# Performance work log

Hardware: AMD Instinct MI355X
Metric: run time of the kernel (lower is better)

Reference implementation:

```python
import jax, jax.numpy as jnp
import numpy as np

N_NODES = 100000
N_EDGES = 200000
IN_FEATS = 1024
H_FEATS = 512
N_HEADS = 4
HEAD_DIM = H_FEATS // N_HEADS  # 128
N_CLASSES = 2983
BATCH = 1024


def setup_inputs() -> dict:
    key = jax.random.key(0)
    ks = jax.random.split(key, 24)
    x = jax.random.normal(ks[0], (N_NODES, IN_FEATS), jnp.float32)
    e1_src = jax.random.randint(ks[1], (N_EDGES,), 0, N_NODES)
    e1_dst = jax.random.randint(ks[2], (N_EDGES,), 0, N_NODES)
    e2_src = jax.random.randint(ks[3], (N_EDGES,), 0, N_NODES)
    e2_dst = jax.random.randint(ks[4], (N_EDGES,), 0, N_NODES)

    def lin_w(k, fin, fout):
        return jax.random.normal(k, (fin, fout), jnp.float32) * np.float32(1.0 / np.sqrt(fin))

    def att_w(k):
        return jax.random.normal(k, (N_HEADS, HEAD_DIM), jnp.float32) * np.float32(0.1)

    inp = dict(x=x, e1_src=e1_src, e1_dst=e1_dst, e2_src=e2_src, e2_dst=e2_dst,
               batch_size=BATCH)
    # layer 0 (in_feats -> h_feats), one GATConv per edge type
    inp["w0a"] = lin_w(ks[5], IN_FEATS, H_FEATS); inp["as0a"] = att_w(ks[6]); inp["ad0a"] = att_w(ks[7]); inp["b0a"] = jnp.zeros((H_FEATS,), jnp.float32)
    inp["w0b"] = lin_w(ks[8], IN_FEATS, H_FEATS); inp["as0b"] = att_w(ks[9]); inp["ad0b"] = att_w(ks[10]); inp["b0b"] = jnp.zeros((H_FEATS,), jnp.float32)
    # layer 1 (h_feats -> h_feats)
    inp["w1a"] = lin_w(ks[11], H_FEATS, H_FEATS); inp["as1a"] = att_w(ks[12]); inp["ad1a"] = att_w(ks[13]); inp["b1a"] = jnp.zeros((H_FEATS,), jnp.float32)
    inp["w1b"] = lin_w(ks[14], H_FEATS, H_FEATS); inp["as1b"] = att_w(ks[15]); inp["ad1b"] = att_w(ks[16]); inp["b1b"] = jnp.zeros((H_FEATS,), jnp.float32)
    # classification head
    inp["lin_w"] = lin_w(ks[17], H_FEATS, N_CLASSES)
    inp["lin_b"] = jnp.zeros((N_CLASSES,), jnp.float32)
    return inp


def gat_conv(x, src, dst, W, a_src, a_dst, b):
    """PyG GATConv (add_self_loops=False, concat=True, attn negative_slope=0.2)."""
    h = (x @ W).reshape(-1, N_HEADS, HEAD_DIM)          # [N, H, C]
    alpha_src = jnp.einsum('nhc,hc->nh', h, a_src)       # [N, H]
    alpha_dst = jnp.einsum('nhc,hc->nh', h, a_dst)       # [N, H]
    e = jax.nn.leaky_relu(alpha_src[src] + alpha_dst[dst], 0.2)   # [E, H]
    # segment softmax over incoming edges of each destination node
    m = jax.ops.segment_max(e, dst, num_segments=N_NODES)          # [N, H]
    ex = jnp.exp(e - m[dst])
    denom = jax.ops.segment_sum(ex, dst, num_segments=N_NODES)     # [N, H]
    alpha = ex / denom[dst]                                        # [E, H]
    msg = alpha[:, :, None] * h[src]                               # [E, H, C]
    out = jax.ops.segment_sum(msg, dst, num_segments=N_NODES)      # [N, H, C]
    return out.reshape(-1, N_HEADS * HEAD_DIM) + b


def reference(x, e1_src, e1_dst, e2_src, e2_dst, batch_size,
              w0a, as0a, ad0a, b0a, w0b, as0b, ad0b, b0b,
              w1a, as1a, ad1a, b1a, w1b, as1b, ad1b, b1b,
              lin_w, lin_b):
    # layer 0: HeteroConv sums per-edge-type GATConv outputs on 'paper'
    h1 = gat_conv(x, e1_src, e1_dst, w0a, as0a, ad0a, b0a) \
       + gat_conv(x, e2_src, e2_dst, w0b, as0b, ad0b, b0b)
    h1 = jax.nn.leaky_relu(h1, 0.01)   # F.leaky_relu default slope; dropout is identity in eval
    # layer 1
    h2 = gat_conv(h1, e1_src, e1_dst, w1a, as1a, ad1a, b1a) \
       + gat_conv(h1, e2_src, e2_dst, w1b, as1b, ad1b, b1b)
    # classification head on the seed nodes
    return h2[:batch_size] @ lin_w + lin_b
```

## Files before the change

### kernel.cpp

```cpp
#include <hip/hip_runtime.h>

#define N_NODES 100000
#define N_EDGES 200000
#define IN_FEATS 1024
#define H_FEATS 512
#define N_HEADS 4
#define HEAD_DIM 128
#define N_CLASSES 2983
#define BATCH 1024

typedef __attribute__((ext_vector_type(8))) short short8;
typedef __attribute__((ext_vector_type(4))) float floatx4;

typedef __attribute__((address_space(1))) void global_as_void;
typedef __attribute__((address_space(3))) void lds_as_void;

__device__ __forceinline__ float bf2f(unsigned short u) {
    union { unsigned int i; float f; } x; x.i = ((unsigned int)u) << 16; return x.f;
}
__device__ __forceinline__ unsigned short f2bf(float f) {
    union { float f; unsigned int i; } x; x.f = f;
    unsigned int r = x.i + 0x7FFFu + ((x.i >> 16) & 1u);
    return (unsigned short)(r >> 16);
}
__device__ __forceinline__ void load_lds16(const void* g, void* l) {
    __builtin_amdgcn_global_load_lds((const global_as_void*)g, (lds_as_void*)l, 16, 0, 0);
}

__global__ __launch_bounds__(256, 3)
void gemm_kernel(const void* __restrict__ Ain, int a_fp32, int a_dense,
                 const unsigned short* __restrict__ BT,
                 void* __restrict__ Cout, const float* __restrict__ bias,
                 const float* __restrict__ att_s, const float* __restrict__ att_d,
                 const float* __restrict__ att_s2, const float* __restrict__ att_d2,
                 float* __restrict__ asrc, float* __restrict__ adst,
                 const int* __restrict__ rowlist, const int* __restrict__ countp,
                 int M, int N, int n_tiles, int K, int out_bf16)
{
    __shared__ __attribute__((aligned(16))) unsigned short As[128 * 32];
    __shared__ __attribute__((aligned(16))) unsigned short Bs[128 * 32];
    const int tid  = threadIdx.x;
    const int lane = tid & 63;
    const int wave = tid >> 6;
    const int bid = blockIdx.x;
    int mt, nt;
    if (n_tiles == 8) {
        int k8 = bid & 7, j = bid >> 3;
        nt = j & 7;
        mt = k8 + ((j >> 3) << 3);
    } else {
        mt = bid / n_tiles;
        nt = bid - mt * n_tiles;
    }
    const int m0 = mt * 128;
    const int n0 = nt * 128;
    int Mv = M;
    if (countp) Mv = countp[0];
    if (m0 >= Mv) return;
    const int wr = (wave >> 1) * 64;
    const int wc = (wave & 1) * 64;
    const int lm = lane & 15;
    const int quad = lane >> 4;

    auto arow = [&](int r) -> int {
        int gr = m0 + r; if (gr > Mv - 1) gr = Mv - 1;
        if (rowlist && !a_dense) gr = rowlist[gr];
        return gr;
    };

    floatx4 acc[4][4];
#pragma unroll
    for (int i = 0; i < 4; i++)
#pragma unroll
        for (int j = 0; j < 4; j++) acc[i][j] = (floatx4)0.0f;

    for (int k0 = 0; k0 < K; k0 += 32) {
        __syncthreads();
        if (a_fp32) {
            int row = tid >> 2;
            int slot = tid & 3;
#pragma unroll
            for (int p = 0; p < 2; p++) {
                int r = p * 64 + row;
                int gr = arow(r);
                int gc = (slot ^ ((r >> 1) & 3)) * 8;
                const float* ap = (const float*)Ain + (size_t)gr * K + k0 + gc;
                floatx4 f0 = *(const floatx4*)ap;
                floatx4 f1 = *(const floatx4*)(ap + 4);
                short8 v;
                v[0] = (short)f2bf(f0[0]); v[1] = (short)f2bf(f0[1]);
                v[2] = (short)f2bf(f0[2]); v[3] = (short)f2bf(f0[3]);
                v[4] = (short)f2bf(f1[0]); v[5] = (short)f2bf(f1[1]);
                v[6] = (short)f2bf(f1[2]); v[7] = (short)f2bf(f1[3]);
                *(short8*)&As[r * 32 + slot * 8] = v;
            }
        } else {
#pragma unroll
            for (int i = 0; i < 2; i++) {
                int r = wave * 32 + i * 16 + (lane >> 2);
                int gr = arow(r);
                int gc = ((lane & 3) ^ ((r >> 1) & 3)) * 8;
                load_lds16((const unsigned short*)Ain + (size_t)gr * K + k0 + gc,
                           (char*)As + (size_t)(wave * 2 + i) * 1024);
            }
        }
#pragma unroll
        for (int i = 0; i < 2; i++) {
            int r = wave * 32 + i * 16 + (lane >> 2);
            int gn = n0 + r; if (gn > N - 1) gn = N - 1;
            int gc = ((lane & 3) ^ ((r >> 1) & 3)) * 8;
            load_lds16(BT + (size_t)gn * K + k0 + gc,
                       (char*)Bs + (size_t)(wave * 2 + i) * 1024);
        }
        __syncthreads();
        short8 af[4], bfr[4];
#pragma unroll
        for (int i = 0; i < 4; i++) {
            int ra = wr + i * 16 + lm;
            af[i] = *(const short8*)&As[ra * 32 + ((quad ^ ((ra >> 1) & 3)) << 3)];
            int rb = wc + i * 16 + lm;
            bfr[i] = *(const short8*)&Bs[rb * 32 + ((quad ^ ((rb >> 1) & 3)) << 3)];
        }
#pragma unroll
        for (int i = 0; i < 4; i++)
#pragma unroll
            for (int j = 0; j < 4; j++)
                acc[i][j] = __builtin_amdgcn_mfma_f32_16x16x32_bf16(af[i], bfr[j], acc[i][j], 0, 0, 0);
    }

    if (att_s) {
        const int h = nt;
        const float* wsp = (h < 4) ? att_s : att_s2;
        const float* wdp = (h < 4) ? att_d : att_d2;
        const int hh = h & 3;
#pragma unroll
        for (int i = 0; i < 4; i++) {
#pragma unroll
            for (int r = 0; r < 4; r++) {
                float ss = 0.f, sd = 0.f;
#pragma unroll
                for (int j = 0; j < 4; j++) {
                    int c = wc + j * 16 + lm;
                    ss += acc[i][j][r] * wsp[hh * HEAD_DIM + c];
                    sd += acc[i][j][r] * wdp[hh * HEAD_DIM + c];
                }
#pragma unroll
                for (int off = 1; off < 16; off <<= 1) {
                    ss += __shfl_xor(ss, off);
                    sd += __shfl_xor(sd, off);
                }
                int grl = m0 + wr + i * 16 + quad * 4 + r;
                if (lm == 0 && grl < Mv) {
                    int gr = rowlist ? rowlist[grl] : grl;
                    atomicAdd(&asrc[(size_t)gr * 8 + h], ss);
                    atomicAdd(&adst[(size_t)gr * 8 + h], sd);
                }
            }
        }
    }

#pragma unroll
    for (int i = 0; i < 4; i++) {
        int grb = wr + i * 16 + quad * 4;
#pragma unroll
        for (int j = 0; j < 4; j++) {
            int gc = n0 + wc + j * 16 + lm;
            if (gc < N) {
#pragma unroll
                for (int r = 0; r < 4; r++) {
                    int grl = m0 + grb + r;
                    if (grl < Mv) {
                        int gr = rowlist ? rowlist[grl] : grl;
                        float v = acc[i][j][r];
                        if (out_bf16) {
                            ((unsigned short*)Cout)[(size_t)gr * N + gc] = f2bf(v);
                        } else {
                            float b = bias ? bias[gc] : 0.0f;
                            ((float*)Cout)[(size_t)gr * N + gc] = v + b;
                        }
                    }
                }
            }
        }
    }
}

__global__ void cvt_rows_kernel(const float* __restrict__ X, const int* __restrict__ list,
                                const int* __restrict__ countp, unsigned short* __restrict__ Y)
{
    int i = blockIdx.x * 2 + (threadIdx.x >> 7);
    if (i >= countp[0]) return;
    int col = (threadIdx.x & 127) * 8;
    const floatx4* xp = (const floatx4*)(X + (size_t)list[i] * IN_FEATS + col);
    floatx4 f0 = xp[0], f1 = xp[1];
    short8 v;
    v[0] = (short)f2bf(f0[0]); v[1] = (short)f2bf(f0[1]);
    v[2] = (short)f2bf(f0[2]); v[3] = (short)f2bf(f0[3]);
    v[4] = (short)f2bf(f1[0]); v[5] = (short)f2bf(f1[1]);
    v[6] = (short)f2bf(f1[2]); v[7] = (short)f2bf(f1[3]);
    *(short8*)(Y + (size_t)i * IN_FEATS + col) = v;
}

__global__ void hist_kernel(const int* __restrict__ dst, int* __restrict__ cnt, int E)
{
    int e = blockIdx.x * blockDim.x + threadIdx.x;
    if (e < E) atomicAdd(&cnt[dst[e]], 1);
}

__global__ void scan1_kernel(const int* __restrict__ cnt, int* __restrict__ partial,
                             int* __restrict__ chunksum, int n)
{
    __shared__ int sm[256];
    int t = threadIdx.x;
    int i = blockIdx.x * 256 + t;
    int v = (i < n) ? cnt[i] : 0;
    sm[t] = v; __syncthreads();
    int val = v;
#pragma unroll
    for (int off = 1; off < 256; off <<= 1) {
        int u = (t >= off) ? sm[t - off] : 0;
        __syncthreads();
        val += u; sm[t] = val;
        __syncthreads();
    }
    if (i < n) partial[i] = val - v;
    if (t == 255) chunksum[blockIdx.x] = val;
}

__global__ void scan2_kernel(int* __restrict__ chunksum, int n)
{
    __shared__ int sm[512];
    int t = threadIdx.x;
    int v = (t < n) ? chunksum[t] : 0;
    sm[t] = v; __syncthreads();
    int val = v;
#pragma unroll
    for (int off = 1; off < 512; off <<= 1) {
        int u = (t >= off) ? sm[t - off] : 0;
        __syncthreads();
        val += u; sm[t] = val;
        __syncthreads();
    }
    if (t < n) chunksum[t] = val - v;
}

__global__ void scan3_kernel(const int* __restrict__ partial, const int* __restrict__ chunksum,
                             int* __restrict__ rowptr, int* __restrict__ cursor, int n, int E)
{
    int i = blockIdx.x * 256 + threadIdx.x;
    if (i < n) {
        int r = partial[i] + chunksum[i >> 8];
        rowptr[i] = r;
        cursor[i] = r;
    }
    if (i == 0) rowptr[n] = E;
}

__global__ void fill_kernel(const int* __restrict__ src, const int* __restrict__ dst,
                            int* __restrict__ cursor, int* __restrict__ srcs_sorted, int E)
{
    int e = blockIdx.x * blockDim.x + threadIdx.x;
    if (e < E) {
        int p = atomicAdd(&cursor[dst[e]], 1);
        srcs_sorted[p] = src[e];
    }
}

__global__ void mark1_kernel(const int* __restrict__ rowptr1, const int* __restrict__ srcs1,
                             const int* __restrict__ rowptr2, const int* __restrict__ srcs2,
                             int* __restrict__ flag, int E)
{
    int e = blockIdx.x * blockDim.x + threadIdx.x;
    if (e >= E) return;
    if (e < BATCH) flag[e] = 1;
    if (e < rowptr1[BATCH]) flag[srcs1[e]] = 1;
    if (e < rowptr2[BATCH]) flag[srcs2[e]] = 1;
}

__global__ void mark0_kernel(const int* __restrict__ e1s, const int* __restrict__ e1d,
                             const int* __restrict__ e2s, const int* __restrict__ e2d,
                             const int* __restrict__ flag1, int* __restrict__ flag0,
                             int E, int Nn)
{
    int i = blockIdx.x * blockDim.x + threadIdx.x;
    if (i < E) {
        if (flag1[e1d[i]]) flag0[e1s[i]] = 1;
        if (flag1[e2d[i]]) flag0[e2s[i]] = 1;
    }
    if (i < Nn && flag1[i]) flag0[i] = 1;
}

__global__ void compact_kernel(const int* __restrict__ flag, const int* __restrict__ partial,
                               const int* __restrict__ chunksum, int* __restrict__ list,
                               int* __restrict__ countp, int n)
{
    int i = blockIdx.x * 256 + threadIdx.x;
    if (i >= n) return;
    int pos = partial[i] + chunksum[i >> 8];
    if (flag[i]) list[pos] = i;
    if (i == n - 1) countp[0] = pos + flag[i];
}

__global__ void gather2_kernel(const int* __restrict__ rowptr1, const int* __restrict__ srcs1,
                               const int* __restrict__ rowptr2, const int* __restrict__ srcs2,
                               const float* __restrict__ asrc, const float* __restrict__ adst,
                               const unsigned short* __restrict__ H,
                               const float* __restrict__ b1, const float* __restrict__ b2,
                               const int* __restrict__ dlist, const int* __restrict__ dcountp,
                               unsigned short* __restrict__ Out, int ndst, int do_lrelu)
{
    int i = blockIdx.x * 4 + (threadIdx.x >> 6);
    int nd = dcountp ? dcountp[0] : ndst;
    if (i >= nd) return;
    int d = dlist ? dlist[i] : i;
    int lane = threadIdx.x & 63;
    int head = lane >> 4;
    int col = lane * 8;
    float r[8], acc[8];
    {
        int beg = rowptr1[d], end = rowptr1[d + 1];
        float ad = adst[(size_t)d * 8 + head];
        float den = 0.f;
#pragma unroll
        for (int k = 0; k < 8; k++) acc[k] = 0.f;
        for (int j = beg; j < end; j++) {
            int s = srcs1[j];
            float v = asrc[(size_t)s * 8 + head] + ad;
            v = v > 0.f ? v : 0.2f * v;
            float ex = expf(v);
            den += ex;
            short8 hv = *(const short8*)(H + (size_t)s * 1024 + col);
#pragma unroll
            for (int k = 0; k < 8; k++) acc[k] += ex * bf2f((unsigned short)hv[k]);
        }
        float inv = den > 0.f ? 1.f / den : 0.f;
#pragma unroll
        for (int k = 0; k < 8; k++) r[k] = acc[k] * inv;
    }
    {
        int beg = rowptr2[d], end = rowptr2[d + 1];
        float ad = adst[(size_t)d * 8 + 4 + head];
        float den = 0.f;
#pragma unroll
        for (int k = 0; k < 8; k++) acc[k] = 0.f;
        for (int j = beg; j < end; j++) {
            int s = srcs2[j];
            float v = asrc[(size_t)s * 8 + 4 + head] + ad;
            v = v > 0.f ? v : 0.2f * v;
            float ex = expf(v);
            den += ex;
            short8 hv = *(const short8*)(H + (size_t)s * 1024 + 512 + col);
#pragma unroll
            for (int k = 0; k < 8; k++) acc[k] += ex * bf2f((unsigned short)hv[k]);
        }
        float inv = den > 0.f ? 1.f / den : 0.f;
#pragma unroll
        for (int k = 0; k < 8; k++) r[k] += acc[k] * inv;
    }
    short8 o;
#pragma unroll
    for (int k = 0; k < 8; k++) {
        float f = r[k] + b1[col + k] + b2[col + k];
        if (do_lrelu) f = f > 0.f ? f : 0.01f * f;
        o[k] = (short)f2bf(f);
    }
    *(short8*)(Out + (size_t)i * 512 + col) = o;
}

__global__ void transpose_conv_kernel(const float* __restrict__ W, unsigned short* __restrict__ WT,
                                      int K, int N)
{
    int idx = blockIdx.x * blockDim.x + threadIdx.x;
    if (idx >= K * N) return;
    int n = idx / K, k = idx - n * K;
    WT[idx] = f2bf(W[(size_t)k * N + n]);
}

extern "C" void kernel_launch(void* const* d_in, const int* in_sizes, int n_in,
                              void* d_out, int out_size, void* d_ws, size_t ws_size,
                              hipStream_t stream)
{
    const float* x    = (const float*)d_in[0];
    const int* e1s    = (const int*)d_in[1];
    const int* e1d    = (const int*)d_in[2];
    const int* e2s    = (const int*)d_in[3];
    const int* e2d    = (const int*)d_in[4];
    const float* w0a  = (const float*)d_in[6];
    const float* as0a = (const float*)d_in[7];
    const float* ad0a = (const float*)d_in[8];
    const float* b0a  = (const float*)d_in[9];
    const float* w0b  = (const float*)d_in[10];
    const float* as0b = (const float*)d_in[11];
    const float* ad0b = (const float*)d_in[12];
    const float* b0b  = (const float*)d_in[13];
    const float* w1a  = (const float*)d_in[14];
    const float* as1a = (const float*)d_in[15];
    const float* ad1a = (const float*)d_in[16];
    const float* b1a  = (const float*)d_in[17];
    const float* w1b  = (const float*)d_in[18];
    const float* as1b = (const float*)d_in[19];
    const float* ad1b = (const float*)d_in[20];
    const float* b1b  = (const float*)d_in[21];
    const float* linw = (const float*)d_in[22];
    const float* linb = (const float*)d_in[23];
    float* out = (float*)d_out;
    (void)in_sizes; (void)n_in; (void)out_size;

    char* ws = (char*)d_ws;
    size_t off = 0;
    auto carve = [&](size_t bytes) -> void* {
        void* p = ws + off; off += (bytes + 255) & ~(size_t)255; return p;
    };
    unsigned short* WT0 = (unsigned short*)carve((size_t)2 * H_FEATS * IN_FEATS * 2);
    unsigned short* WT1 = (unsigned short*)carve((size_t)2 * H_FEATS * H_FEATS * 2);
    unsigned short* WTl = (unsigned short*)carve((size_t)N_CLASSES * H_FEATS * 2);
    unsigned short* Hbf = (unsigned short*)carve((size_t)N_NODES * 1024 * 2);
    unsigned short* H1c = (unsigned short*)carve((size_t)N_NODES * H_FEATS * 2);
    unsigned short* h2s = (unsigned short*)carve((size_t)BATCH * H_FEATS * 2);
    float* asrc = (float*)carve((size_t)N_NODES * 8 * 4);
    float* adst = (float*)carve((size_t)N_NODES * 8 * 4);
    int* rowptr1 = (int*)carve((size_t)(N_NODES + 1) * 4);
    int* rowptr2 = (int*)carve((size_t)(N_NODES + 1) * 4);
    int* srcs1   = (int*)carve((size_t)N_EDGES * 4);
    int* srcs2   = (int*)carve((size_t)N_EDGES * 4);
    int* cnt     = (int*)carve((size_t)N_NODES * 4);
    int* partial = (int*)carve((size_t)N_NODES * 4);
    int* chunksum= (int*)carve((size_t)512 * 4);
    int* flag1   = (int*)carve((size_t)N_NODES * 4);
    int* flag0   = (int*)carve((size_t)N_NODES * 4);
    int* list1   = (int*)carve((size_t)N_NODES * 4);
    int* list0   = (int*)carve((size_t)N_NODES * 4);
    int* count1  = (int*)carve(256);
    int* count0  = (int*)carve(256);
    unsigned short* xc = nullptr;
    {
        size_t need = (size_t)N_NODES * IN_FEATS * 2;
        if (off + need <= ws_size) xc = (unsigned short*)carve(need);
    }

    const int NCHUNK = (N_NODES + 255) / 256;
    const int MT8 = (((N_NODES + 127) / 128) + 7) & ~7;

    {
        int t0 = IN_FEATS * H_FEATS;
        transpose_conv_kernel<<<(t0 + 255) / 256, 256, 0, stream>>>(w0a, WT0, IN_FEATS, H_FEATS);
        transpose_conv_kernel<<<(t0 + 255) / 256, 256, 0, stream>>>(w0b, WT0 + (size_t)H_FEATS * IN_FEATS, IN_FEATS, H_FEATS);
        int t1 = H_FEATS * H_FEATS;
        transpose_conv_kernel<<<(t1 + 255) / 256, 256, 0, stream>>>(w1a, WT1, H_FEATS, H_FEATS);
        transpose_conv_kernel<<<(t1 + 255) / 256, 256, 0, stream>>>(w1b, WT1 + (size_t)H_FEATS * H_FEATS, H_FEATS, H_FEATS);
        int t2 = H_FEATS * N_CLASSES;
        transpose_conv_kernel<<<(t2 + 255) / 256, 256, 0, stream>>>(linw, WTl, H_FEATS, N_CLASSES);
    }

    auto build_csr = [&](const int* src, const int* dst, int* rowptr, int* srcs_sorted) {
        hipMemsetAsync(cnt, 0, (size_t)N_NODES * 4, stream);
        hist_kernel<<<(N_EDGES + 255) / 256, 256, 0, stream>>>(dst, cnt, N_EDGES);
        scan1_kernel<<<NCHUNK, 256, 0, stream>>>(cnt, partial, chunksum, N_NODES);
        scan2_kernel<<<1, 512, 0, stream>>>(chunksum, NCHUNK);
        scan3_kernel<<<NCHUNK, 256, 0, stream>>>(partial, chunksum, rowptr, cnt, N_NODES, N_EDGES);
        fill_kernel<<<(N_EDGES + 255) / 256, 256, 0, stream>>>(src, dst, cnt, srcs_sorted, N_EDGES);
    };
    build_csr(e1s, e1d, rowptr1, srcs1);
    build_csr(e2s, e2d, rowptr2, srcs2);

    hipMemsetAsync(flag1, 0, (size_t)N_NODES * 4, stream);
    mark1_kernel<<<(N_EDGES + 255) / 256, 256, 0, stream>>>(rowptr1, srcs1, rowptr2, srcs2, flag1, N_EDGES);
    scan1_kernel<<<NCHUNK, 256, 0, stream>>>(flag1, partial, chunksum, N_NODES);
    scan2_kernel<<<1, 512, 0, stream>>>(chunksum, NCHUNK);
    compact_kernel<<<NCHUNK, 256, 0, stream>>>(flag1, partial, chunksum, list1, count1, N_NODES);

    hipMemsetAsync(flag0, 0, (size_t)N_NODES * 4, stream);
    mark0_kernel<<<(N_EDGES + 255) / 256, 256, 0, stream>>>(e1s, e1d, e2s, e2d, flag1, flag0, N_EDGES, N_NODES);
    scan1_kernel<<<NCHUNK, 256, 0, stream>>>(flag0, partial, chunksum, N_NODES);
    scan2_kernel<<<1, 512, 0, stream>>>(chunksum, NCHUNK);
    compact_kernel<<<NCHUNK, 256, 0, stream>>>(flag0, partial, chunksum, list0, count0, N_NODES);

    if (xc) {
        cvt_rows_kernel<<<(N_NODES + 1) / 2, 256, 0, stream>>>(x, list0, count0, xc);
    }

    hipMemsetAsync(asrc, 0, (size_t)N_NODES * 8 * 4, stream);
    hipMemsetAsync(adst, 0, (size_t)N_NODES * 8 * 4, stream);
    if (xc) {
        gemm_kernel<<<MT8 * 8, 256, 0, stream>>>(xc, 0, 1, WT0, Hbf, nullptr,
                                                 as0a, ad0a, as0b, ad0b, asrc, adst,
                                                 list0, count0,
                                                 N_NODES, 1024, 8, IN_FEATS, 1);
    } else {
        gemm_kernel<<<MT8 * 8, 256, 0, stream>>>(x, 1, 0, WT0, Hbf, nullptr,
                                                 as0a, ad0a, as0b, ad0b, asrc, adst,
                                                 list0, count0,
                                                 N_NODES, 1024, 8, IN_FEATS, 1);
    }
    gather2_kernel<<<(N_NODES + 3) / 4, 256, 0, stream>>>(rowptr1, srcs1, rowptr2, srcs2,
                                                          asrc, adst, Hbf, b0a, b0b,
                                                          list1, count1,
                                                          H1c, N_NODES, 1);

    hipMemsetAsync(asrc, 0, (size_t)N_NODES * 8 * 4, stream);
    hipMemsetAsync(adst, 0, (size_t)N_NODES * 8 * 4, stream);
    gemm_kernel<<<MT8 * 8, 256, 0, stream>>>(H1c, 0, 1, WT1, Hbf, nullptr,
                                             as1a, ad1a, as1b, ad1b, asrc, adst,
                                             list1, count1,
                                             N_NODES, 1024, 8, H_FEATS, 1);
    gather2_kernel<<<(BATCH + 3) / 4, 256, 0, stream>>>(rowptr1, srcs1, rowptr2, srcs2,
                                                        asrc, adst, Hbf, b1a, b1b,
                                                        nullptr, nullptr,
                                                        h2s, BATCH, 0);

    const int HN_T = (N_CLASSES + 127) / 128;
    gemm_kernel<<<(BATCH / 128) * HN_T, 256, 0, stream>>>(h2s, 0, 0, WTl, out, linb,
                                                          nullptr, nullptr, nullptr, nullptr,
                                                          nullptr, nullptr, nullptr, nullptr,
                                                          BATCH, N_CLASSES, HN_T, H_FEATS, 0);
}
```

Measured before the change: 850.9 us.

## Merge CSR builds and frontier compaction, replace attention atomics with LDS reduction

Builds both edge-type CSRs in one combined histogram/scan/fill pass and computes both frontier flag sets in a single scan and compaction. The five weight transposes become three batched launches, and gather and convert kernels switch to fixed-size grid-stride grids. In the GEMM, per-thread load pointers are hoisted out of the K loop. The attention-logit atomics are replaced with an LDS reduction followed by plain stores, which removes the asrc/adst memsets. The goal is fewer launches and memsets and less atomic traffic, at the cost of a larger single-block scan and an extra barrier in the GEMM epilogue.

```diff
diff --git a/kernel.cpp b/kernel.cpp
--- a/kernel.cpp
+++ b/kernel.cpp
@@ -39,15 +39,15 @@
 {
     __shared__ __attribute__((aligned(16))) unsigned short As[128 * 32];
     __shared__ __attribute__((aligned(16))) unsigned short Bs[128 * 32];
+    __shared__ float attbuf[128][4];
     const int tid  = threadIdx.x;
     const int lane = tid & 63;
     const int wave = tid >> 6;
     const int bid = blockIdx.x;
     int mt, nt;
     if (n_tiles == 8) {
-        int k8 = bid & 7, j = bid >> 3;
-        nt = j & 7;
-        mt = k8 + ((j >> 3) << 3);
+        mt = (bid & 7) + ((bid >> 6) << 3);
+        nt = (bid >> 3) & 7;
     } else {
         mt = bid / n_tiles;
         nt = bid - mt * n_tiles;
@@ -68,6 +68,35 @@
         return gr;
     };
 
+    const float* a_fp[2];
+    const unsigned short* a_bf[2];
+    char* a_lds[2];
+    const unsigned short* b_bf[2];
+    char* b_lds[2];
+    if (a_fp32) {
+        int row = tid >> 2, slot = tid & 3;
+#pragma unroll
+        for (int p = 0; p < 2; p++) {
+            int r = p * 64 + row;
+            a_fp[p] = (const float*)Ain + (size_t)arow(r) * K + (slot ^ ((r >> 1) & 3)) * 8;
+        }
+    } else {
+#pragma unroll
+        for (int i = 0; i < 2; i++) {
+            int r = wave * 32 + i * 16 + (lane >> 2);
+            a_bf[i] = (const unsigned short*)Ain + (size_t)arow(r) * K
+                    + ((lane & 3) ^ ((r >> 1) & 3)) * 8;
+            a_lds[i] = (char*)As + (size_t)(wave * 2 + i) * 1024;
+        }
+    }
+#pragma unroll
+    for (int i = 0; i < 2; i++) {
+        int r = wave * 32 + i * 16 + (lane >> 2);
+        int gn = n0 + r; if (gn > N - 1) gn = N - 1;
+        b_bf[i] = BT + (size_t)gn * K + ((lane & 3) ^ ((r >> 1) & 3)) * 8;
+        b_lds[i] = (char*)Bs + (size_t)(wave * 2 + i) * 1024;
+    }
+
     floatx4 acc[4][4];
 #pragma unroll
     for (int i = 0; i < 4; i++)
@@ -77,16 +106,12 @@
     for (int k0 = 0; k0 < K; k0 += 32) {
         __syncthreads();
         if (a_fp32) {
-            int row = tid >> 2;
-            int slot = tid & 3;
+            int row = tid >> 2, slot = tid & 3;
 #pragma unroll
             for (int p = 0; p < 2; p++) {
                 int r = p * 64 + row;
-                int gr = arow(r);
-                int gc = (slot ^ ((r >> 1) & 3)) * 8;
-                const float* ap = (const float*)Ain + (size_t)gr * K + k0 + gc;
-                floatx4 f0 = *(const floatx4*)ap;
-                floatx4 f1 = *(const floatx4*)(ap + 4);
+                floatx4 f0 = *(const floatx4*)(a_fp[p] + k0);
+                floatx4 f1 = *(const floatx4*)(a_fp[p] + k0 + 4);
                 short8 v;
                 v[0] = (short)f2bf(f0[0]); v[1] = (short)f2bf(f0[1]);
                 v[2] = (short)f2bf(f0[2]); v[3] = (short)f2bf(f0[3]);
@@ -96,22 +121,12 @@
             }
         } else {
 #pragma unroll
-            for (int i = 0; i < 2; i++) {
-                int r = wave * 32 + i * 16 + (lane >> 2);
-                int gr = arow(r);
-                int gc = ((lane & 3) ^ ((r >> 1) & 3)) * 8;
-                load_lds16((const unsigned short*)Ain + (size_t)gr * K + k0 + gc,
-                           (char*)As + (size_t)(wave * 2 + i) * 1024);
-            }
-        }
-#pragma unroll
-        for (int i = 0; i < 2; i++) {
-            int r = wave * 32 + i * 16 + (lane >> 2);
-            int gn = n0 + r; if (gn > N - 1) gn = N - 1;
-            int gc = ((lane & 3) ^ ((r >> 1) & 3)) * 8;
-            load_lds16(BT + (size_t)gn * K + k0 + gc,
-                       (char*)Bs + (size_t)(wave * 2 + i) * 1024);
-        }
+            for (int i = 0; i < 2; i++)
+                load_lds16(a_bf[i] + k0, a_lds[i]);
+        }
+#pragma unroll
+        for (int i = 0; i < 2; i++)
+            load_lds16(b_bf[i] + k0, b_lds[i]);
         __syncthreads();
         short8 af[4], bfr[4];
 #pragma unroll
@@ -133,6 +148,7 @@
         const float* wsp = (h < 4) ? att_s : att_s2;
         const float* wdp = (h < 4) ? att_d : att_d2;
         const int hh = h & 3;
+        const int half2 = (wc >> 6) * 2;
 #pragma unroll
         for (int i = 0; i < 4; i++) {
 #pragma unroll
@@ -149,12 +165,20 @@
                     ss += __shfl_xor(ss, off);
                     sd += __shfl_xor(sd, off);
                 }
-                int grl = m0 + wr + i * 16 + quad * 4 + r;
-                if (lm == 0 && grl < Mv) {
-                    int gr = rowlist ? rowlist[grl] : grl;
-                    atomicAdd(&asrc[(size_t)gr * 8 + h], ss);
-                    atomicAdd(&adst[(size_t)gr * 8 + h], sd);
+                if (lm == 0) {
+                    int rl = wr + i * 16 + quad * 4 + r;
+                    attbuf[rl][half2]     = ss;
+                    attbuf[rl][half2 + 1] = sd;
                 }
+            }
+        }
+        __syncthreads();
+        if (tid < 128) {
+            int grl = m0 + tid;
+            if (grl < Mv) {
+                int gr = rowlist ? rowlist[grl] : grl;
+                asrc[(size_t)gr * 8 + h] = attbuf[tid][0] + attbuf[tid][2];
+                adst[(size_t)gr * 8 + h] = attbuf[tid][1] + attbuf[tid][3];
             }
         }
     }
@@ -188,23 +212,28 @@
 __global__ void cvt_rows_kernel(const float* __restrict__ X, const int* __restrict__ list,
                                 const int* __restrict__ countp, unsigned short* __restrict__ Y)
 {
-    int i = blockIdx.x * 2 + (threadIdx.x >> 7);
-    if (i >= countp[0]) return;
+    int n0 = countp[0];
     int col = (threadIdx.x & 127) * 8;
-    const floatx4* xp = (const floatx4*)(X + (size_t)list[i] * IN_FEATS + col);
-    floatx4 f0 = xp[0], f1 = xp[1];
-    short8 v;
-    v[0] = (short)f2bf(f0[0]); v[1] = (short)f2bf(f0[1]);
-    v[2] = (short)f2bf(f0[2]); v[3] = (short)f2bf(f0[3]);
-    v[4] = (short)f2bf(f1[0]); v[5] = (short)f2bf(f1[1]);
-    v[6] = (short)f2bf(f1[2]); v[7] = (short)f2bf(f1[3]);
-    *(short8*)(Y + (size_t)i * IN_FEATS + col) = v;
-}
-
-__global__ void hist_kernel(const int* __restrict__ dst, int* __restrict__ cnt, int E)
+    for (int i = blockIdx.x * 2 + (threadIdx.x >> 7); i < n0; i += gridDim.x * 2) {
+        const floatx4* xp = (const floatx4*)(X + (size_t)list[i] * IN_FEATS + col);
+        floatx4 f0 = xp[0], f1 = xp[1];
+        short8 v;
+        v[0] = (short)f2bf(f0[0]); v[1] = (short)f2bf(f0[1]);
+        v[2] = (short)f2bf(f0[2]); v[3] = (short)f2bf(f0[3]);
+        v[4] = (short)f2bf(f1[0]); v[5] = (short)f2bf(f1[1]);
+        v[6] = (short)f2bf(f1[2]); v[7] = (short)f2bf(f1[3]);
+        *(short8*)(Y + (size_t)i * IN_FEATS + col) = v;
+    }
+}
+
+__global__ void hist2_kernel(const int* __restrict__ e1d, const int* __restrict__ e2d,
+                             int* __restrict__ cnt2, int E)
 {
     int e = blockIdx.x * blockDim.x + threadIdx.x;
-    if (e < E) atomicAdd(&cnt[dst[e]], 1);
+    if (e < E) {
+        atomicAdd(&cnt2[e1d[e]], 1);
+        atomicAdd(&cnt2[N_NODES + e2d[e]], 1);
+    }
 }
 
 __global__ void scan1_kernel(const int* __restrict__ cnt, int* __restrict__ partial,
@@ -229,13 +258,13 @@
 
 __global__ void scan2_kernel(int* __restrict__ chunksum, int n)
 {
-    __shared__ int sm[512];
+    __shared__ int sm[1024];
     int t = threadIdx.x;
     int v = (t < n) ? chunksum[t] : 0;
     sm[t] = v; __syncthreads();
     int val = v;
 #pragma unroll
-    for (int off = 1; off < 512; off <<= 1) {
+    for (int off = 1; off < 1024; off <<= 1) {
         int u = (t >= off) ? sm[t - off] : 0;
         __syncthreads();
         val += u; sm[t] = val;
@@ -244,37 +273,40 @@
     if (t < n) chunksum[t] = val - v;
 }
 
-__global__ void scan3_kernel(const int* __restrict__ partial, const int* __restrict__ chunksum,
-                             int* __restrict__ rowptr, int* __restrict__ cursor, int n, int E)
+__global__ void scan3c_kernel(const int* __restrict__ partial, const int* __restrict__ chunksum,
+                              int* __restrict__ rowptrc, int* __restrict__ cursor, int n, int Etot)
 {
     int i = blockIdx.x * 256 + threadIdx.x;
     if (i < n) {
         int r = partial[i] + chunksum[i >> 8];
-        rowptr[i] = r;
+        rowptrc[i] = r;
         cursor[i] = r;
     }
-    if (i == 0) rowptr[n] = E;
-}
-
-__global__ void fill_kernel(const int* __restrict__ src, const int* __restrict__ dst,
-                            int* __restrict__ cursor, int* __restrict__ srcs_sorted, int E)
+    if (i == 0) rowptrc[n] = Etot;
+}
+
+__global__ void fill2_kernel(const int* __restrict__ e1s, const int* __restrict__ e1d,
+                             const int* __restrict__ e2s, const int* __restrict__ e2d,
+                             int* __restrict__ cursor, int* __restrict__ srcsc, int E)
 {
     int e = blockIdx.x * blockDim.x + threadIdx.x;
     if (e < E) {
-        int p = atomicAdd(&cursor[dst[e]], 1);
-        srcs_sorted[p] = src[e];
-    }
-}
-
-__global__ void mark1_kernel(const int* __restrict__ rowptr1, const int* __restrict__ srcs1,
-                             const int* __restrict__ rowptr2, const int* __restrict__ srcs2,
-                             int* __restrict__ flag, int E)
+        int p = atomicAdd(&cursor[e1d[e]], 1);
+        srcsc[p] = e1s[e];
+        int q = atomicAdd(&cursor[N_NODES + e2d[e]], 1);
+        srcsc[q] = e2s[e];
+    }
+}
+
+__global__ void mark1_kernel(const int* __restrict__ e1s, const int* __restrict__ e1d,
+                             const int* __restrict__ e2s, const int* __restrict__ e2d,
+                             int* __restrict__ flag1, int E)
 {
     int e = blockIdx.x * blockDim.x + threadIdx.x;
     if (e >= E) return;
-    if (e < BATCH) flag[e] = 1;
-    if (e < rowptr1[BATCH]) flag[srcs1[e]] = 1;
-    if (e < rowptr2[BATCH]) flag[srcs2[e]] = 1;
+    if (e < BATCH) flag1[e] = 1;
+    if (e1d[e] < BATCH) flag1[e1s[e]] = 1;
+    if (e2d[e] < BATCH) flag1[e2s[e]] = 1;
 }
 
 __global__ void mark0_kernel(const int* __restrict__ e1s, const int* __restrict__ e1d,
@@ -290,90 +322,98 @@
     if (i < Nn && flag1[i]) flag0[i] = 1;
 }
 
-__global__ void compact_kernel(const int* __restrict__ flag, const int* __restrict__ partial,
-                               const int* __restrict__ chunksum, int* __restrict__ list,
-                               int* __restrict__ countp, int n)
+__global__ void compactF_kernel(const int* __restrict__ flag, const int* __restrict__ partial,
+                                const int* __restrict__ chunksum,
+                                int* __restrict__ list1, int* __restrict__ list0,
+                                int* __restrict__ count1, int* __restrict__ count0)
 {
     int i = blockIdx.x * 256 + threadIdx.x;
-    if (i >= n) return;
+    if (i >= 2 * N_NODES) return;
+    int total1 = partial[N_NODES] + chunksum[N_NODES >> 8];
     int pos = partial[i] + chunksum[i >> 8];
-    if (flag[i]) list[pos] = i;
-    if (i == n - 1) countp[0] = pos + flag[i];
-}
-
-__global__ void gather2_kernel(const int* __restrict__ rowptr1, const int* __restrict__ srcs1,
-                               const int* __restrict__ rowptr2, const int* __restrict__ srcs2,
+    if (i < N_NODES) {
+        if (flag[i]) list1[pos] = i;
+        if (i == 0) count1[0] = total1;
+    } else {
+        if (flag[i]) list0[pos - total1] = i - N_NODES;
+        if (i == 2 * N_NODES - 1) count0[0] = pos + flag[i] - total1;
+    }
+}
+
+__global__ void gather2_kernel(const int* __restrict__ rowptrc, const int* __restrict__ srcsc,
                                const float* __restrict__ asrc, const float* __restrict__ adst,
                                const unsigned short* __restrict__ H,
                                const float* __restrict__ b1, const float* __restrict__ b2,
                                const int* __restrict__ dlist, const int* __restrict__ dcountp,
                                unsigned short* __restrict__ Out, int ndst, int do_lrelu)
 {
-    int i = blockIdx.x * 4 + (threadIdx.x >> 6);
     int nd = dcountp ? dcountp[0] : ndst;
-    if (i >= nd) return;
-    int d = dlist ? dlist[i] : i;
     int lane = threadIdx.x & 63;
     int head = lane >> 4;
     int col = lane * 8;
-    float r[8], acc[8];
-    {
-        int beg = rowptr1[d], end = rowptr1[d + 1];
-        float ad = adst[(size_t)d * 8 + head];
-        float den = 0.f;
-#pragma unroll
-        for (int k = 0; k < 8; k++) acc[k] = 0.f;
-        for (int j = beg; j < end; j++) {
-            int s = srcs1[j];
-            float v = asrc[(size_t)s * 8 + head] + ad;
-            v = v > 0.f ? v : 0.2f * v;
-            float ex = expf(v);
-            den += ex;
-            short8 hv = *(const short8*)(H + (size_t)s * 1024 + col);
-#pragma unroll
-            for (int k = 0; k < 8; k++) acc[k] += ex * bf2f((unsigned short)hv[k]);
-        }
-        float inv = den > 0.f ? 1.f / den : 0.f;
-#pragma unroll
-        for (int k = 0; k < 8; k++) r[k] = acc[k] * inv;
-    }
-    {
-        int beg = rowptr2[d], end = rowptr2[d + 1];
-        float ad = adst[(size_t)d * 8 + 4 + head];
-        float den = 0.f;
-#pragma unroll
-        for (int k = 0; k < 8; k++) acc[k] = 0.f;
-        for (int j = beg; j < end; j++) {
-            int s = srcs2[j];
-            float v = asrc[(size_t)s * 8 + 4 + head] + ad;
-            v = v > 0.f ? v : 0.2f * v;
-            float ex = expf(v);
-            den += ex;
-            short8 hv = *(const short8*)(H + (size_t)s * 1024 + 512 + col);
-#pragma unroll
-            for (int k = 0; k < 8; k++) acc[k] += ex * bf2f((unsigned short)hv[k]);
-        }
-        float inv = den > 0.f ? 1.f / den : 0.f;
-#pragma unroll
-        for (int k = 0; k < 8; k++) r[k] += acc[k] * inv;
-    }
-    short8 o;
-#pragma unroll
-    for (int k = 0; k < 8; k++) {
-        float f = r[k] + b1[col + k] + b2[col + k];
-        if (do_lrelu) f = f > 0.f ? f : 0.01f * f;
-        o[k] = (short)f2bf(f);
-    }
-    *(short8*)(Out + (size_t)i * 512 + col) = o;
-}
-
-__global__ void transpose_conv_kernel(const float* __restrict__ W, unsigned short* __restrict__ WT,
-                                      int K, int N)
-{
-    int idx = blockIdx.x * blockDim.x + threadIdx.x;
-    if (idx >= K * N) return;
-    int n = idx / K, k = idx - n * K;
-    WT[idx] = f2bf(W[(size_t)k * N + n]);
+    for (int i = blockIdx.x * 4 + (threadIdx.x >> 6); i < nd; i += gridDim.x * 4) {
+        int d = dlist ? dlist[i] : i;
+        float r[8], acc[8];
+        {
+            int beg = rowptrc[d], end = rowptrc[d + 1];
+            float ad = adst[(size_t)d * 8 + head];
+            float den = 0.f;
+#pragma unroll
+            for (int k = 0; k < 8; k++) acc[k] = 0.f;
+            for (int j = beg; j < end; j++) {
+                int s = srcsc[j];
+                float v = asrc[(size_t)s * 8 + head] + ad;
+                v = v > 0.f ? v : 0.2f * v;
+                float ex = expf(v);
+                den += ex;
+                short8 hv = *(const short8*)(H + (size_t)s * 1024 + col);
+#pragma unroll
+                for (int k = 0; k < 8; k++) acc[k] += ex * bf2f((unsigned short)hv[k]);
+            }
+            float inv = den > 0.f ? 1.f / den : 0.f;
+#pragma unroll
+            for (int k = 0; k < 8; k++) r[k] = acc[k] * inv;
+        }
+        {
+            int beg = rowptrc[N_NODES + d], end = rowptrc[N_NODES + d + 1];
+            float ad = adst[(size_t)d * 8 + 4 + head];
+            float den = 0.f;
+#pragma unroll
+            for (int k = 0; k < 8; k++) acc[k] = 0.f;
+            for (int j = beg; j < end; j++) {
+                int s = srcsc[j];
+                float v = asrc[(size_t)s * 8 + 4 + head] + ad;
+                v = v > 0.f ? v : 0.2f * v;
+                float ex = expf(v);
+                den += ex;
+                short8 hv = *(const short8*)(H + (size_t)s * 1024 + 512 + col);
+#pragma unroll
+                for (int k = 0; k < 8; k++) acc[k] += ex * bf2f((unsigned short)hv[k]);
+            }
+            float inv = den > 0.f ? 1.f / den : 0.f;
+#pragma unroll
+            for (int k = 0; k < 8; k++) r[k] += acc[k] * inv;
+        }
+        short8 o;
+#pragma unroll
+        for (int k = 0; k < 8; k++) {
+            float f = r[k] + b1[col + k] + b2[col + k];
+            if (do_lrelu) f = f > 0.f ? f : 0.01f * f;
+            o[k] = (short)f2bf(f);
+        }
+        *(short8*)(Out + (size_t)i * 512 + col) = o;
+    }
+}
+
+__global__ void transpose2_kernel(const float* __restrict__ Wa, const float* __restrict__ Wb,
+                                  unsigned short* __restrict__ WT, int K, int Nh)
+{
+    int k = blockIdx.x * 256 + threadIdx.x;
+    if (k >= K) return;
+    int n = blockIdx.y;
+    const float* W = (n < Nh) ? Wa : Wb;
+    int nn = (n < Nh) ? n : n - Nh;
+    WT[(size_t)n * K + k] = f2bf(W[(size_t)k * Nh + nn]);
 }
 
 extern "C" void kernel_launch(void* const* d_in, const int* in_sizes, int n_in,
@@ -419,15 +459,12 @@
     unsigned short* h2s = (unsigned short*)carve((size_t)BATCH * H_FEATS * 2);
     float* asrc = (float*)carve((size_t)N_NODES * 8 * 4);
     float* adst = (float*)carve((size_t)N_NODES * 8 * 4);
-    int* rowptr1 = (int*)carve((size_t)(N_NODES + 1) * 4);
-    int* rowptr2 = (int*)carve((size_t)(N_NODES + 1) * 4);
-    int* srcs1   = (int*)carve((size_t)N_EDGES * 4);
-    int* srcs2   = (int*)carve((size_t)N_EDGES * 4);
-    int* cnt     = (int*)carve((size_t)N_NODES * 4);
-    int* partial = (int*)carve((size_t)N_NODES * 4);
-    int* chunksum= (int*)carve((size_t)512 * 4);
-    int* flag1   = (int*)carve((size_t)N_NODES * 4);
-    int* flag0   = (int*)carve((size_t)N_NODES * 4);
+    int* rowptrc = (int*)carve((size_t)(2 * N_NODES + 1) * 4);
+    int* srcsc   = (int*)carve((size_t)2 * N_EDGES * 4);
+    int* cnt2    = (int*)carve((size_t)2 * N_NODES * 4);
+    int* partial = (int*)carve((size_t)2 * N_NODES * 4);
+    int* chunksum= (int*)carve((size_t)1024 * 4);
+    int* flagbuf = (int*)carve((size_t)2 * N_NODES * 4);
     int* list1   = (int*)carve((size_t)N_NODES * 4);
     int* list0   = (int*)carve((size_t)N_NODES * 4);
     int* count1  = (int*)carve(256);
@@ -438,49 +475,35 @@
         if (off + need <= ws_size) xc = (unsigned short*)carve(need);
     }
 
-    const int NCHUNK = (N_NODES + 255) / 256;
+    const int NCHUNK2 = (2 * N_NODES + 255) / 256;
     const int MT8 = (((N_NODES + 127) / 128) + 7) & ~7;
-
-    {
-        int t0 = IN_FEATS * H_FEATS;
-        transpose_conv_kernel<<<(t0 + 255) / 256, 256, 0, stream>>>(w0a, WT0, IN_FEATS, H_FEATS);
-        transpose_conv_kernel<<<(t0 + 255) / 256, 256, 0, stream>>>(w0b, WT0 + (size_t)H_FEATS * IN_FEATS, IN_FEATS, H_FEATS);
-        int t1 = H_FEATS * H_FEATS;
-        transpose_conv_kernel<<<(t1 + 255) / 256, 256, 0, stream>>>(w1a, WT1, H_FEATS, H_FEATS);
-        transpose_conv_kernel<<<(t1 + 255) / 256, 256, 0, stream>>>(w1b, WT1 + (size_t)H_FEATS * H_FEATS, H_FEATS, H_FEATS);
-        int t2 = H_FEATS * N_CLASSES;
-        transpose_conv_kernel<<<(t2 + 255) / 256, 256, 0, stream>>>(linw, WTl, H_FEATS, N_CLASSES);
-    }
-
-    auto build_csr = [&](const int* src, const int* dst, int* rowptr, int* srcs_sorted) {
-        hipMemsetAsync(cnt, 0, (size_t)N_NODES * 4, stream);
-        hist_kernel<<<(N_EDGES + 255) / 256, 256, 0, stream>>>(dst, cnt, N_EDGES);
-        scan1_kernel<<<NCHUNK, 256, 0, stream>>>(cnt, partial, chunksum, N_NODES);
-        scan2_kernel<<<1, 512, 0, stream>>>(chunksum, NCHUNK);
-        scan3_kernel<<<NCHUNK, 256, 0, stream>>>(partial, chunksum, rowptr, cnt, N_NODES, N_EDGES);
-        fill_kernel<<<(N_EDGES + 255) / 256, 256, 0, stream>>>(src, dst, cnt, srcs_sorted, N_EDGES);
-    };
-    build_csr(e1s, e1d, rowptr1, srcs1);
-    build_csr(e2s, e2d, rowptr2, srcs2);
-
-    hipMemsetAsync(flag1, 0, (size_t)N_NODES * 4, stream);
-    mark1_kernel<<<(N_EDGES + 255) / 256, 256, 0, stream>>>(rowptr1, srcs1, rowptr2, srcs2, flag1, N_EDGES);
-    scan1_kernel<<<NCHUNK, 256, 0, stream>>>(flag1, partial, chunksum, N_NODES);
-    scan2_kernel<<<1, 512, 0, stream>>>(chunksum, NCHUNK);
-    compact_kernel<<<NCHUNK, 256, 0, stream>>>(flag1, partial, chunksum, list1, count1, N_NODES);
-
-    hipMemsetAsync(flag0, 0, (size_t)N_NODES * 4, stream);
-    mark0_kernel<<<(N_EDGES + 255) / 256, 256, 0, stream>>>(e1s, e1d, e2s, e2d, flag1, flag0, N_EDGES, N_NODES);
-    scan1_kernel<<<NCHUNK, 256, 0, stream>>>(flag0, partial, chunksum, N_NODES);
-    scan2_kernel<<<1, 512, 0, stream>>>(chunksum, NCHUNK);
-    compact_kernel<<<NCHUNK, 256, 0, stream>>>(flag0, partial, chunksum, list0, count0, N_NODES);
+    const int EG = (N_EDGES + 255) / 256;
+
+    transpose2_kernel<<<dim3(IN_FEATS / 256, 2 * H_FEATS), 256, 0, stream>>>(w0a, w0b, WT0, IN_FEATS, H_FEATS);
+    transpose2_kernel<<<dim3(H_FEATS / 256, 2 * H_FEATS), 256, 0, stream>>>(w1a, w1b, WT1, H_FEATS, H_FEATS);
+    transpose2_kernel<<<dim3(H_FEATS / 256, N_CLASSES), 256, 0, stream>>>(linw, linw, WTl, H_FEATS, N_CLASSES);
+
+    hipMemsetAsync(flagbuf, 0, (size_t)2 * N_NODES * 4, stream);
+    mark1_kernel<<<EG, 256, 0, stream>>>(e1s, e1d, e2s, e2d, flagbuf, N_EDGES);
+    mark0_kernel<<<EG, 256, 0, stream>>>(e1s, e1d, e2s, e2d, flagbuf, flagbuf + N_NODES,
+                                         N_EDGES, N_NODES);
+    scan1_kernel<<<NCHUNK2, 256, 0, stream>>>(flagbuf, partial, chunksum, 2 * N_NODES);
+    scan2_kernel<<<1, 1024, 0, stream>>>(chunksum, NCHUNK2);
+    compactF_kernel<<<NCHUNK2, 256, 0, stream>>>(flagbuf, partial, chunksum,
+                                                 list1, list0, count1, count0);
+
+    hipMemsetAsync(cnt2, 0, (size_t)2 * N_NODES * 4, stream);
+    hist2_kernel<<<EG, 256, 0, stream>>>(e1d, e2d, cnt2, N_EDGES);
+    scan1_kernel<<<NCHUNK2, 256, 0, stream>>>(cnt2, partial, chunksum, 2 * N_NODES);
+    scan2_kernel<<<1, 1024, 0, stream>>>(chunksum, NCHUNK2);
+    scan3c_kernel<<<NCHUNK2, 256, 0, stream>>>(partial, chunksum, rowptrc, cnt2,
+                                               2 * N_NODES, 2 * N_EDGES);
+    fill2_kernel<<<EG, 256, 0, stream>>>(e1s, e1d, e2s, e2d, cnt2, srcsc, N_EDGES);
 
     if (xc) {
-        cvt_rows_kernel<<<(N_NODES + 1) / 2, 256, 0, stream>>>(x, list0, count0, xc);
-    }
-
-    hipMemsetAsync(asrc, 0, (size_t)N_NODES * 8 * 4, stream);
-    hipMemsetAsync(adst, 0, (size_t)N_NODES * 8 * 4, stream);
+        cvt_rows_kernel<<<1024, 256, 0, stream>>>(x, list0, count0, xc);
+    }
+
     if (xc) {
         gemm_kernel<<<MT8 * 8, 256, 0, stream>>>(xc, 0, 1, WT0, Hbf, nullptr,
                                                  as0a, ad0a, as0b, ad0b, asrc, adst,
@@ -492,21 +515,15 @@
                                                  list0, count0,
                                                  N_NODES, 1024, 8, IN_FEATS, 1);
     }
-    gather2_kernel<<<(N_NODES + 3) / 4, 256, 0, stream>>>(rowptr1, srcs1, rowptr2, srcs2,
-                                                          asrc, adst, Hbf, b0a, b0b,
-                                                          list1, count1,
-                                                          H1c, N_NODES, 1);
-
-    hipMemsetAsync(asrc, 0, (size_t)N_NODES * 8 * 4, stream);
-    hipMemsetAsync(adst, 0, (size_t)N_NODES * 8 * 4, stream);
+    gather2_kernel<<<2048, 256, 0, stream>>>(rowptrc, srcsc, asrc, adst, Hbf, b0a, b0b,
+                                             list1, count1, H1c, N_NODES, 1);
+
     gemm_kernel<<<MT8 * 8, 256, 0, stream>>>(H1c, 0, 1, WT1, Hbf, nullptr,
                                              as1a, ad1a, as1b, ad1b, asrc, adst,
                                              list1, count1,
                                              N_NODES, 1024, 8, H_FEATS, 1);
-    gather2_kernel<<<(BATCH + 3) / 4, 256, 0, stream>>>(rowptr1, srcs1, rowptr2, srcs2,
-                                                        asrc, adst, Hbf, b1a, b1b,
-                                                        nullptr, nullptr,
-                                                        h2s, BATCH, 0);
+    gather2_kernel<<<256, 256, 0, stream>>>(rowptrc, srcsc, asrc, adst, Hbf, b1a, b1b,
+                                            nullptr, nullptr, h2s, BATCH, 0);
 
     const int HN_T = (N_CLASSES + 127) / 128;
     gemm_kernel<<<(BATCH / 128) * HN_T, 256, 0, stream>>>(h2s, 0, 0, WTl, out, linb,
```

Result: faster. 775.8 us (-8.8%).
